# Kernel tuning notes

Hardware: AMD Instinct MI355X
Metric: run time of the kernel (lower is better)

## Reference

```python
import jax, jax.numpy as jnp
import numpy as np

B = 8192
MOTION_DIM = 512
COMMAND_DIM = 64
HIDDEN = 1024
E = 8  # num_experts
NUM_LAYERS = 6


def _dense(key, shape, fan_in):
    return jax.random.normal(key, shape, dtype=jnp.float32) * (1.0 / np.sqrt(fan_in))


def setup_inputs() -> dict:
    key = jax.random.key(0)
    ks = jax.random.split(key, 32)
    in_dim = MOTION_DIM + COMMAND_DIM  # 576
    inp = {
        "motion": jax.random.normal(ks[0], (B, MOTION_DIM), dtype=jnp.float32),
        "command": jax.random.normal(ks[1], (B, COMMAND_DIM), dtype=jnp.float32),
        # gating network: in -> H -> H -> E, ELU, softmax
        "g_w1": _dense(ks[2], (in_dim, HIDDEN), in_dim),
        "g_b1": jnp.zeros((HIDDEN,), jnp.float32),
        "g_w2": _dense(ks[3], (HIDDEN, HIDDEN), HIDDEN),
        "g_b2": jnp.zeros((HIDDEN,), jnp.float32),
        "g_w3": _dense(ks[4], (HIDDEN, E), HIDDEN),
        "g_b3": jnp.zeros((E,), jnp.float32),
        # MoE layers: dims [in->H, H->H, H->H, H->H, H->H?, ...] per CMG layout
        "w0": _dense(ks[5], (E, in_dim, HIDDEN), in_dim),
        "b0": jnp.zeros((E, HIDDEN), jnp.float32),
        "w1": _dense(ks[6], (E, HIDDEN, HIDDEN), HIDDEN),
        "b1": jnp.zeros((E, HIDDEN), jnp.float32),
        "w2": _dense(ks[7], (E, HIDDEN, HIDDEN), HIDDEN),
        "b2": jnp.zeros((E, HIDDEN), jnp.float32),
        "w3": _dense(ks[8], (E, HIDDEN, HIDDEN), HIDDEN),
        "b3": jnp.zeros((E, HIDDEN), jnp.float32),
        "w4": _dense(ks[9], (E, HIDDEN, HIDDEN), HIDDEN),
        "b4": jnp.zeros((E, HIDDEN), jnp.float32),
        "w5": _dense(ks[10], (E, HIDDEN, MOTION_DIM), HIDDEN),
        "b5": jnp.zeros((E, MOTION_DIM), jnp.float32),
    }
    return inp


def _moe_layer(x, coeffs, W, b):
    # x: [B, din], coeffs: [B, E], W: [E, din, dout], b: [E, dout]
    # y[b] = sum_e coeffs[b,e] * (x[b] @ W[e] + b[e])
    y = jnp.einsum("be,bi,eio->bo", coeffs, x, W)
    y = y + jnp.einsum("be,eo->bo", coeffs, b)
    return y


def _cmg_forward(motion, command,
                 g_w1, g_b1, g_w2, g_b2, g_w3, g_b3,
                 w0, b0, w1, b1, w2, b2, w3, b3, w4, b4, w5, b5):
    x = jnp.concatenate([motion, command], axis=-1)  # [B, in_dim]
    # gating network
    g = jax.nn.elu(x @ g_w1 + g_b1)
    g = jax.nn.elu(g @ g_w2 + g_b2)
    coeffs = jax.nn.softmax(g @ g_w3 + g_b3, axis=-1)  # [B, E]
    # stacked MoE layers with ELU between all but last
    Ws = [w0, w1, w2, w3, w4, w5]
    bs = [b0, b1, b2, b3, b4, b5]
    for i in range(NUM_LAYERS):
        x = _moe_layer(x, coeffs, Ws[i], bs[i])
        if i < NUM_LAYERS - 1:
            x = jax.nn.elu(x)
    return x  # [B, MOTION_DIM]


def reference(motion, command,
              g_w1, g_b1, g_w2, g_b2, g_w3, g_b3,
              w0, b0, w1, b1, w2, b2, w3, b3, w4, b4, w5, b5):
    return _cmg_forward(motion, command,
                        g_w1, g_b1, g_w2, g_b2, g_w3, g_b3,
                        w0, b0, w1, b1, w2, b2, w3, b3, w4, b4, w5, b5)
```

## Files before the change

### kernel.cpp

```cpp
#include <hip/hip_runtime.h>
#include <hip/hip_bf16.h>

typedef __attribute__((ext_vector_type(8))) short bf16x8;
typedef __attribute__((ext_vector_type(4))) float f32x4;

__device__ __forceinline__ float bf2f(unsigned short u) {
    union { unsigned int i; float f; } v; v.i = ((unsigned int)u) << 16; return v.f;
}
__device__ __forceinline__ unsigned short f2bf(float f) {
    union { float f; unsigned int i; } v; v.f = f;
    unsigned int x = v.i;
    return (unsigned short)((x + 0x7FFFu + ((x >> 16) & 1u)) >> 16);
}

__device__ __forceinline__ void gload_lds16(const unsigned short* g, unsigned short* l) {
    __builtin_amdgcn_global_load_lds(
        (const __attribute__((address_space(1))) unsigned int*)g,
        (__attribute__((address_space(3))) unsigned int*)l,
        16, 0, 0);
}

#define VM0  asm volatile("s_waitcnt vmcnt(0)" ::: "memory")
#define SB0  __builtin_amdgcn_sched_barrier(0)
#define BAR  __builtin_amdgcn_s_barrier()

__global__ void concat_cvt(const float* __restrict__ motion,
                           const float* __restrict__ command,
                           unsigned short* __restrict__ out) {
    int id = blockIdx.x * 256 + threadIdx.x;
    int b = id / 144, q = id % 144;
    float4 v;
    if (q < 128) v = *(const float4*)(motion + (size_t)b * 512 + q * 4);
    else         v = *(const float4*)(command + (size_t)b * 64 + (q - 128) * 4);
    ushort4 o;
    o.x = f2bf(v.x); o.y = f2bf(v.y); o.z = f2bf(v.z); o.w = f2bf(v.w);
    *(ushort4*)(out + (size_t)b * 576 + q * 4) = o;
}

__global__ void transpose_cvt(const float* __restrict__ in,
                              unsigned short* __restrict__ out,
                              int K, int N, int tpe) {
    __shared__ unsigned short tile[64][72];
    int e = blockIdx.x / tpe, r = blockIdx.x % tpe;
    in  += (size_t)e * K * N;
    out += (size_t)e * N * K;
    int nbn = N / 64;
    int k0 = (r / nbn) * 64;
    int n0 = (r % nbn) * 64;
    int t = threadIdx.x;
    int tx = t & 63, ty = t >> 6;
    #pragma unroll
    for (int rr = 0; rr < 16; ++rr) {
        int kr = ty + rr * 4;
        tile[kr][tx] = f2bf(in[(size_t)(k0 + kr) * N + n0 + tx]);
    }
    __syncthreads();
    int txh = t & 31, tyh = t >> 5;
    #pragma unroll
    for (int rr = 0; rr < 8; ++rr) {
        int nr = tyh + rr * 8;
        unsigned int vlo = tile[2 * txh][nr];
        unsigned int vhi = tile[2 * txh + 1][nr];
        unsigned int* o32 = (unsigned int*)(out + (size_t)(n0 + nr) * K + k0);
        o32[txh] = vlo | (vhi << 16);
    }
}

__global__ __launch_bounds__(256) void gating_kernel(
    const unsigned short* __restrict__ g2,
    const float* __restrict__ w3, const float* __restrict__ b3,
    float* __restrict__ coeffs) {
    __shared__ float w3s[8][1024];
    int t = threadIdx.x;
    for (int i = t; i < 1024; i += 256) {
        #pragma unroll
        for (int e = 0; e < 8; ++e) w3s[e][i] = w3[(size_t)i * 8 + e];
    }
    __syncthreads();
    int lane = t & 63, wv = t >> 6;
    int row = blockIdx.x * 4 + wv;
    const unsigned short* xr = g2 + (size_t)row * 1024;
    float acc[8];
    #pragma unroll
    for (int e = 0; e < 8; ++e) acc[e] = 0.f;
    for (int it = 0; it < 16; ++it) {
        float xv = bf2f(xr[lane + it * 64]);
        #pragma unroll
        for (int e = 0; e < 8; ++e) acc[e] += xv * w3s[e][lane + it * 64];
    }
    #pragma unroll
    for (int e = 0; e < 8; ++e) {
        float v = acc[e];
        #pragma unroll
        for (int off = 32; off; off >>= 1) v += __shfl_xor(v, off);
        acc[e] = v + b3[e];
    }
    float mx = acc[0];
    #pragma unroll
    for (int e = 1; e < 8; ++e) mx = fmaxf(mx, acc[e]);
    float s = 0.f;
    #pragma unroll
    for (int e = 0; e < 8; ++e) { acc[e] = __expf(acc[e] - mx); s += acc[e]; }
    float inv = 1.f / s;
    if (lane < 8) coeffs[(size_t)row * 8 + lane] = acc[lane] * inv;
}

template<bool DO_ELU>
__global__ __launch_bounds__(256, 4)
void gemm_bf16(const unsigned short* __restrict__ A,
               const unsigned short* __restrict__ BT,
               const float* __restrict__ bias,
               unsigned short* __restrict__ Out,
               int N, int ld, int kpart) {
    __shared__ unsigned short As[128 * 64];
    __shared__ unsigned short Bs[128 * 64];
    int ntn = N >> 7;
    int nwg = gridDim.x;
    int bid = blockIdx.x;
    { int cpx = nwg >> 3; bid = (bid & 7) * cpx + (bid >> 3); }
    int tm = bid / ntn, tn = bid - tm * ntn;
    int row0 = tm << 7, col0 = tn << 7;
    int t = threadIdx.x;
    int lane = t & 63;
    int wid = t >> 6;
    int wr = wid >> 1, wc = wid & 1;
    const unsigned short* Ab = A + (size_t)(row0 + wid * 32 + (lane >> 3)) * ld + (lane & 7) * 8;
    const unsigned short* Bb = BT + (size_t)(col0 + wid * 32 + (lane >> 3)) * ld + (lane & 7) * 8;
    unsigned short* Asd = &As[wid * 32 * 64];
    unsigned short* Bsd = &Bs[wid * 32 * 64];
    f32x4 acc[4][4];
    #pragma unroll
    for (int i = 0; i < 4; ++i)
        #pragma unroll
        for (int j = 0; j < 4; ++j) acc[i][j] = (f32x4){0.f, 0.f, 0.f, 0.f};
    int nkt = kpart >> 6;
    for (int kt = 0; kt < nkt; ++kt) {
        size_t ko = (size_t)kt << 6;
        #pragma unroll
        for (int q = 0; q < 4; ++q) {
            gload_lds16(Ab + (size_t)(q * 8) * ld + ko, Asd + q * 8 * 64);
            gload_lds16(Bb + (size_t)(q * 8) * ld + ko, Bsd + q * 8 * 64);
        }
        __syncthreads();
        #pragma unroll
        for (int kk = 0; kk < 2; ++kk) {
            bf16x8 af[4], bfr[4];
            #pragma unroll
            for (int m = 0; m < 4; ++m)
                af[m] = *(const bf16x8*)(&As[(wr * 64 + m * 16 + (lane & 15)) * 64 + kk * 32 + (lane >> 4) * 8]);
            #pragma unroll
            for (int n = 0; n < 4; ++n)
                bfr[n] = *(const bf16x8*)(&Bs[(wc * 64 + n * 16 + (lane & 15)) * 64 + kk * 32 + (lane >> 4) * 8]);
            #pragma unroll
            for (int m = 0; m < 4; ++m)
                #pragma unroll
                for (int n = 0; n < 4; ++n)
                    acc[m][n] = __builtin_amdgcn_mfma_f32_16x16x32_bf16(af[m], bfr[n], acc[m][n], 0, 0, 0);
        }
        __syncthreads();
    }
    #pragma unroll
    for (int m = 0; m < 4; ++m) {
        int rbase = row0 + wr * 64 + m * 16 + ((lane >> 4) << 2);
        #pragma unroll
        for (int n = 0; n < 4; ++n) {
            int cg = col0 + wc * 64 + n * 16 + (lane & 15);
            float bv = bias[cg];
            #pragma unroll
            for (int r2 = 0; r2 < 4; ++r2) {
                float v = acc[m][n][r2] + bv;
                if (DO_ELU) v = v > 0.f ? v : (__expf(v) - 1.f);
                Out[(size_t)(rbase + r2) * N + cg] = f2bf(v);
            }
        }
    }
}

template<bool DO_ELU, bool OUT_F32>
__global__ __launch_bounds__(512, 1)
void gemm_fused(const unsigned short* __restrict__ A,
                const unsigned short* __restrict__ BT,
                const float* __restrict__ coeffs,
                const float* __restrict__ bias,
                void* __restrict__ Out,
                int K, int dout) {
    __shared__ unsigned short lds[65536];

    int bid = blockIdx.x;
    int x = bid & 7;
    int i = bid >> 3;
    int within = i & 15;
    int tm = x * 4 + (within & 3);
    int tn = (i >> 4) * 4 + (within >> 2);
    int row0 = tm << 8;
    int c0 = tn << 5;
    int nkt = K >> 5;

    int t = threadIdx.x;
    int lane = t & 63, wid = t >> 6;
    int wm = wid >> 2, wn = wid & 3;
    int q = lane >> 4;
    int l15 = lane & 15;

    int aoff[8], boff[4];
    #pragma unroll
    for (int m = 0; m < 8; ++m) {
        int row = wm * 128 + m * 16 + l15;
        aoff[m] = row * 32 + ((q ^ ((row >> 1) & 3)) << 3);
    }
    #pragma unroll
    for (int n = 0; n < 4; ++n) {
        int row = wn * 64 + n * 16 + l15;
        boff[n] = 8192 + row * 32 + ((q ^ ((row >> 1) & 3)) << 3);
    }

    int srow = t >> 2;
    int scol = ((t & 3) ^ ((t >> 3) & 3)) * 8;
    const unsigned short* Asrc = A + (size_t)(row0 + srow) * K + scol;
    int br0 = (srow >> 5) * dout + c0 + (srow & 31);
    int br1 = ((srow + 128) >> 5) * dout + c0 + (srow & 31);
    const unsigned short* Bsrc0 = BT + (size_t)br0 * K + scol;
    const unsigned short* Bsrc1 = BT + (size_t)br1 * K + scol;
    int wdst = wid * 512;

    f32x4 acc[8][4];
    #pragma unroll
    for (int m = 0; m < 8; ++m)
        #pragma unroll
        for (int n = 0; n < 4; ++n) acc[m][n] = (f32x4){0.f, 0.f, 0.f, 0.f};

    #pragma unroll
    for (int S = 0; S < 2; ++S) {
        gload_lds16(Asrc + S * 32,                   &lds[S * 16384 + wdst]);
        gload_lds16(Asrc + (size_t)128 * K + S * 32, &lds[S * 16384 + 4096 + wdst]);
        gload_lds16(Bsrc0 + S * 32,                  &lds[S * 16384 + 8192 + wdst]);
        gload_lds16(Bsrc1 + S * 32,                  &lds[S * 16384 + 12288 + wdst]);
    }

    for (int s = 0; s < nkt; s += 2) {
        int sbA = (s & 3) << 14;
        int sbB = ((s + 1) & 3) << 14;
        bool st = (s + 2) < nkt;

        VM0; SB0;
        BAR;
        if (st) {
            int rbA = ((s + 2) & 3) << 14;
            int rbB = ((s + 3) & 3) << 14;
            int koA = (s + 2) << 5;
            int koB = (s + 3) << 5;
            gload_lds16(Asrc + koA,                   &lds[rbA + wdst]);
            gload_lds16(Asrc + (size_t)128 * K + koA, &lds[rbA + 4096 + wdst]);
            gload_lds16(Bsrc0 + koA,                  &lds[rbA + 8192 + wdst]);
            gload_lds16(Bsrc1 + koA,                  &lds[rbA + 12288 + wdst]);
            gload_lds16(Asrc + koB,                   &lds[rbB + wdst]);
            gload_lds16(Asrc + (size_t)128 * K + koB, &lds[rbB + 4096 + wdst]);
            gload_lds16(Bsrc0 + koB,                  &lds[rbB + 8192 + wdst]);
            gload_lds16(Bsrc1 + koB,                  &lds[rbB + 12288 + wdst]);
        }
        SB0;

        {
            bf16x8 bfrg[4], afr[8];
            #pragma unroll
            for (int n = 0; n < 4; ++n)
                bfrg[n] = *(const bf16x8*)(&lds[sbA + boff[n]]);
            #pragma unroll
            for (int m = 0; m < 8; ++m)
                afr[m] = *(const bf16x8*)(&lds[sbA + aoff[m]]);
            __builtin_amdgcn_s_setprio(1);
            #pragma unroll
            for (int m = 0; m < 8; ++m)
                #pragma unroll
                for (int n = 0; n < 4; ++n)
                    acc[m][n] = __builtin_amdgcn_mfma_f32_16x16x32_bf16(bfrg[n], afr[m], acc[m][n], 0, 0, 0);
            __builtin_amdgcn_s_setprio(0);
        }
        {
            bf16x8 bfrg[4], afr[8];
            #pragma unroll
            for (int n = 0; n < 4; ++n)
                bfrg[n] = *(const bf16x8*)(&lds[sbB + boff[n]]);
            #pragma unroll
            for (int m = 0; m < 8; ++m)
                afr[m] = *(const bf16x8*)(&lds[sbB + aoff[m]]);
            __builtin_amdgcn_s_setprio(1);
            #pragma unroll
            for (int m = 0; m < 8; ++m)
                #pragma unroll
                for (int n = 0; n < 4; ++n)
                    acc[m][n] = __builtin_amdgcn_mfma_f32_16x16x32_bf16(bfrg[n], afr[m], acc[m][n], 0, 0, 0);
            __builtin_amdgcn_s_setprio(0);
        }
        SB0;
    }

    float* plds = (float*)lds;
    __syncthreads();
    {
        int e0 = 2 * wn, e1 = e0 + 1;
        f32x4 b0h[2], b1h[2];
        #pragma unroll
        for (int h = 0; h < 2; ++h) {
            float4 u0 = *(const float4*)(bias + e0 * dout + c0 + h * 16 + q * 4);
            float4 u1 = *(const float4*)(bias + e1 * dout + c0 + h * 16 + q * 4);
            b0h[h] = (f32x4){u0.x, u0.y, u0.z, u0.w};
            b1h[h] = (f32x4){u1.x, u1.y, u1.z, u1.w};
        }
        float* preg = plds + (wid << 12);
        #pragma unroll
        for (int m = 0; m < 8; ++m) {
            int grow = row0 + wm * 128 + m * 16 + l15;
            float c8 = coeffs[(size_t)grow * 8 + e0];
            float c9 = coeffs[(size_t)grow * 8 + e1];
            #pragma unroll
            for (int h = 0; h < 2; ++h) {
                f32x4 z0 = acc[m][h];
                f32x4 z1 = acc[m][h + 2];
                f32x4 p;
                #pragma unroll
                for (int r = 0; r < 4; ++r)
                    p[r] = c8 * (z0[r] + b0h[h][r]) + c9 * (z1[r] + b1h[h][r]);
                int row = m * 16 + l15;
                int slot = (h * 4 + q) ^ (row & 7);
                *(f32x4*)(preg + row * 32 + (slot << 2)) = p;
            }
        }
    }
    __syncthreads();

    {
        int r2 = t >> 1;
        int ch = t & 1;
        int wmr = r2 >> 7;
        int rr = r2 & 127;
        int sw = rr & 7;
        size_t obase = (size_t)(row0 + r2) * dout + c0 + ch * 16;
        #pragma unroll
        for (int sl = 0; sl < 4; ++sl) {
            int L = ch * 4 + sl;
            int phys = L ^ sw;
            f32x4 sum = (f32x4){0.f, 0.f, 0.f, 0.f};
            #pragma unroll
            for (int w2 = 0; w2 < 4; ++w2) {
                const f32x4 v = *(const f32x4*)(plds + (((wmr << 2) + w2) << 12) + rr * 32 + (phys << 2));
                sum[0] += v[0]; sum[1] += v[1]; sum[2] += v[2]; sum[3] += v[3];
            }
            if (DO_ELU) {
                #pragma unroll
                for (int r = 0; r < 4; ++r)
                    sum[r] = sum[r] > 0.f ? sum[r] : (__expf(sum[r]) - 1.f);
            }
            if (OUT_F32) {
                float4 o = {sum[0], sum[1], sum[2], sum[3]};
                *(float4*)((float*)Out + obase + sl * 4) = o;
            } else {
                ushort4 o;
                o.x = f2bf(sum[0]); o.y = f2bf(sum[1]);
                o.z = f2bf(sum[2]); o.w = f2bf(sum[3]);
                *(ushort4*)((unsigned short*)Out + obase + sl * 4) = o;
            }
        }
    }
}

extern "C" void kernel_launch(void* const* d_in, const int* in_sizes, int n_in,
                              void* d_out, int out_size, void* d_ws, size_t ws_size,
                              hipStream_t stream) {
    const float* motion  = (const float*)d_in[0];
    const float* command = (const float*)d_in[1];
    const float* g_w1 = (const float*)d_in[2];
    const float* g_b1 = (const float*)d_in[3];
    const float* g_w2 = (const float*)d_in[4];
    const float* g_b2 = (const float*)d_in[5];
    const float* g_w3 = (const float*)d_in[6];
    const float* g_b3 = (const float*)d_in[7];
    const float* w[6]  = {(const float*)d_in[8],  (const float*)d_in[10],
                          (const float*)d_in[12], (const float*)d_in[14],
                          (const float*)d_in[16], (const float*)d_in[18]};
    const float* bb[6] = {(const float*)d_in[9],  (const float*)d_in[11],
                          (const float*)d_in[13], (const float*)d_in[15],
                          (const float*)d_in[17], (const float*)d_in[19]};

    char* ws = (char*)d_ws;
    unsigned short* xc0  = (unsigned short*)ws;
    unsigned short* actA = (unsigned short*)(ws + 9437184);
    unsigned short* actB = (unsigned short*)(ws + 26214400);
    float* coeffs        = (float*)(ws + 42991616);
    unsigned short* wT   = (unsigned short*)(ws + 43253760);

    concat_cvt<<<4608, 256, 0, stream>>>(motion, command, xc0);

    transpose_cvt<<<144, 256, 0, stream>>>(g_w1, wT, 576, 1024, 144);
    gemm_bf16<true><<<512, 256, 0, stream>>>(xc0, wT, g_b1, actA, 1024, 576, 576);
    transpose_cvt<<<256, 256, 0, stream>>>(g_w2, wT, 1024, 1024, 256);
    gemm_bf16<true><<<512, 256, 0, stream>>>(actA, wT, g_b2, actB, 1024, 1024, 1024);
    gating_kernel<<<2048, 256, 0, stream>>>(actB, g_w3, g_b3, coeffs);

    transpose_cvt<<<1152, 256, 0, stream>>>(w[0], wT, 576, 1024, 144);
    gemm_fused<true, false><<<1024, 512, 0, stream>>>(
        xc0, wT, coeffs, bb[0], actA, 576, 1024);

    unsigned short* bufs[2] = {actA, actB};
    for (int l = 1; l <= 4; ++l) {
        unsigned short* in  = bufs[(l + 1) & 1];
        unsigned short* out = bufs[l & 1];
        transpose_cvt<<<2048, 256, 0, stream>>>(w[l], wT, 1024, 1024, 256);
        gemm_fused<true, false><<<1024, 512, 0, stream>>>(
            in, wT, coeffs, bb[l], out, 1024, 1024);
    }

    transpose_cvt<<<1024, 256, 0, stream>>>(w[5], wT, 1024, 512, 128);
    gemm_fused<false, true><<<512, 512, 0, stream>>>(
        actA, wT, coeffs, bb[5], d_out, 1024, 512);
}
```

Before: 736.0 us.

## Load B fragments directly to registers and pipeline A through LDS per k-step

The B operand (expert weight tiles) is now read straight from global memory into registers in MFMA fragment layout, double-buffered across k-steps, rather than staged through LDS. Only A tiles are still staged in LDS, using a 4-slot ring with partial vmcnt waits and one barrier per 32-wide k-step instead of full drains every two steps. This cuts LDS traffic and space for B and lets loads overlap compute more finely. In exchange it adds more frequent barriers, uncoalesced per-lane 16-byte global reads for B, and higher register pressure.

```diff
diff --git a/kernel.cpp b/kernel.cpp
--- a/kernel.cpp
+++ b/kernel.cpp
@@ -20,6 +20,8 @@
         16, 0, 0);
 }
 
+#define VM2  asm volatile("s_waitcnt vmcnt(2)" ::: "memory")
+#define VM6  asm volatile("s_waitcnt vmcnt(6)" ::: "memory")
 #define VM0  asm volatile("s_waitcnt vmcnt(0)" ::: "memory")
 #define SB0  __builtin_amdgcn_sched_barrier(0)
 #define BAR  __builtin_amdgcn_s_barrier()
@@ -202,98 +204,87 @@
     int q = lane >> 4;
     int l15 = lane & 15;
 
-    int aoff[8], boff[4];
+    int aoff[8];
     #pragma unroll
     for (int m = 0; m < 8; ++m) {
         int row = wm * 128 + m * 16 + l15;
         aoff[m] = row * 32 + ((q ^ ((row >> 1) & 3)) << 3);
     }
-    #pragma unroll
-    for (int n = 0; n < 4; ++n) {
-        int row = wn * 64 + n * 16 + l15;
-        boff[n] = 8192 + row * 32 + ((q ^ ((row >> 1) & 3)) << 3);
-    }
 
     int srow = t >> 2;
     int scol = ((t & 3) ^ ((t >> 3) & 3)) * 8;
     const unsigned short* Asrc = A + (size_t)(row0 + srow) * K + scol;
-    int br0 = (srow >> 5) * dout + c0 + (srow & 31);
-    int br1 = ((srow + 128) >> 5) * dout + c0 + (srow & 31);
-    const unsigned short* Bsrc0 = BT + (size_t)br0 * K + scol;
-    const unsigned short* Bsrc1 = BT + (size_t)br1 * K + scol;
     int wdst = wid * 512;
 
+    const unsigned short* Bp[4];
+    #pragma unroll
+    for (int n = 0; n < 4; ++n) {
+        int e = 2 * wn + (n >> 1);
+        int j = (n & 1) * 16 + l15;
+        Bp[n] = BT + (size_t)(e * dout + c0 + j) * K + q * 8;
+    }
+
     f32x4 acc[8][4];
     #pragma unroll
     for (int m = 0; m < 8; ++m)
         #pragma unroll
         for (int n = 0; n < 4; ++n) acc[m][n] = (f32x4){0.f, 0.f, 0.f, 0.f};
 
-    #pragma unroll
-    for (int S = 0; S < 2; ++S) {
-        gload_lds16(Asrc + S * 32,                   &lds[S * 16384 + wdst]);
-        gload_lds16(Asrc + (size_t)128 * K + S * 32, &lds[S * 16384 + 4096 + wdst]);
-        gload_lds16(Bsrc0 + S * 32,                  &lds[S * 16384 + 8192 + wdst]);
-        gload_lds16(Bsrc1 + S * 32,                  &lds[S * 16384 + 12288 + wdst]);
+    uint4 bA0, bA1, bA2, bA3, bB0, bB1, bB2, bB3;
+
+    gload_lds16(Asrc,                    &lds[wdst]);
+    gload_lds16(Asrc + (size_t)128 * K,  &lds[4096 + wdst]);
+    gload_lds16(Asrc + 32,                   &lds[8192 + wdst]);
+    gload_lds16(Asrc + (size_t)128 * K + 32, &lds[8192 + 4096 + wdst]);
+    bA0 = *(const uint4*)(Bp[0]);
+    bA1 = *(const uint4*)(Bp[1]);
+    bA2 = *(const uint4*)(Bp[2]);
+    bA3 = *(const uint4*)(Bp[3]);
+    VM6; SB0;
+    BAR;
+
+    #define SLOT_BODY(S, CUR0, CUR1, CUR2, CUR3, NX0, NX1, NX2, NX3)            \
+    {                                                                           \
+        int s_ = (S);                                                           \
+        bool st_ = (s_ + 2) < nkt;                                              \
+        if (st_) {                                                              \
+            int rb_ = ((s_ + 2) & 3) << 13;                                     \
+            int ko_ = (s_ + 2) << 5;                                            \
+            gload_lds16(Asrc + ko_,                   &lds[rb_ + wdst]);        \
+            gload_lds16(Asrc + (size_t)128 * K + ko_, &lds[rb_ + 4096 + wdst]); \
+        }                                                                       \
+        if (st_) { VM2; } else { VM0; }                                         \
+        BAR; SB0;                                                               \
+        if ((s_ + 1) < nkt) {                                                   \
+            int kb_ = (s_ + 1) << 5;                                            \
+            NX0 = *(const uint4*)(Bp[0] + kb_);                                 \
+            NX1 = *(const uint4*)(Bp[1] + kb_);                                 \
+            NX2 = *(const uint4*)(Bp[2] + kb_);                                 \
+            NX3 = *(const uint4*)(Bp[3] + kb_);                                 \
+        }                                                                       \
+        int sb_ = (s_ & 3) << 13;                                               \
+        bf16x8 afr_[8];                                                         \
+        _Pragma("unroll")                                                       \
+        for (int m = 0; m < 8; ++m)                                             \
+            afr_[m] = *(const bf16x8*)(&lds[sb_ + aoff[m]]);                    \
+        bf16x8 bf0_ = *(const bf16x8*)&CUR0;                                    \
+        bf16x8 bf1_ = *(const bf16x8*)&CUR1;                                    \
+        bf16x8 bf2_ = *(const bf16x8*)&CUR2;                                    \
+        bf16x8 bf3_ = *(const bf16x8*)&CUR3;                                    \
+        _Pragma("unroll")                                                       \
+        for (int m = 0; m < 8; ++m) {                                           \
+            acc[m][0] = __builtin_amdgcn_mfma_f32_16x16x32_bf16(bf0_, afr_[m], acc[m][0], 0, 0, 0); \
+            acc[m][1] = __builtin_amdgcn_mfma_f32_16x16x32_bf16(bf1_, afr_[m], acc[m][1], 0, 0, 0); \
+            acc[m][2] = __builtin_amdgcn_mfma_f32_16x16x32_bf16(bf2_, afr_[m], acc[m][2], 0, 0, 0); \
+            acc[m][3] = __builtin_amdgcn_mfma_f32_16x16x32_bf16(bf3_, afr_[m], acc[m][3], 0, 0, 0); \
+        }                                                                       \
     }
 
     for (int s = 0; s < nkt; s += 2) {
-        int sbA = (s & 3) << 14;
-        int sbB = ((s + 1) & 3) << 14;
-        bool st = (s + 2) < nkt;
-
-        VM0; SB0;
-        BAR;
-        if (st) {
-            int rbA = ((s + 2) & 3) << 14;
-            int rbB = ((s + 3) & 3) << 14;
-            int koA = (s + 2) << 5;
-            int koB = (s + 3) << 5;
-            gload_lds16(Asrc + koA,                   &lds[rbA + wdst]);
-            gload_lds16(Asrc + (size_t)128 * K + koA, &lds[rbA + 4096 + wdst]);
-            gload_lds16(Bsrc0 + koA,                  &lds[rbA + 8192 + wdst]);
-            gload_lds16(Bsrc1 + koA,                  &lds[rbA + 12288 + wdst]);
-            gload_lds16(Asrc + koB,                   &lds[rbB + wdst]);
-            gload_lds16(Asrc + (size_t)128 * K + koB, &lds[rbB + 4096 + wdst]);
-            gload_lds16(Bsrc0 + koB,                  &lds[rbB + 8192 + wdst]);
-            gload_lds16(Bsrc1 + koB,                  &lds[rbB + 12288 + wdst]);
-        }
-        SB0;
-
-        {
-            bf16x8 bfrg[4], afr[8];
-            #pragma unroll
-            for (int n = 0; n < 4; ++n)
-                bfrg[n] = *(const bf16x8*)(&lds[sbA + boff[n]]);
-            #pragma unroll
-            for (int m = 0; m < 8; ++m)
-                afr[m] = *(const bf16x8*)(&lds[sbA + aoff[m]]);
-            __builtin_amdgcn_s_setprio(1);
-            #pragma unroll
-            for (int m = 0; m < 8; ++m)
-                #pragma unroll
-                for (int n = 0; n < 4; ++n)
-                    acc[m][n] = __builtin_amdgcn_mfma_f32_16x16x32_bf16(bfrg[n], afr[m], acc[m][n], 0, 0, 0);
-            __builtin_amdgcn_s_setprio(0);
-        }
-        {
-            bf16x8 bfrg[4], afr[8];
-            #pragma unroll
-            for (int n = 0; n < 4; ++n)
-                bfrg[n] = *(const bf16x8*)(&lds[sbB + boff[n]]);
-            #pragma unroll
-            for (int m = 0; m < 8; ++m)
-                afr[m] = *(const bf16x8*)(&lds[sbB + aoff[m]]);
-            __builtin_amdgcn_s_setprio(1);
-            #pragma unroll
-            for (int m = 0; m < 8; ++m)
-                #pragma unroll
-                for (int n = 0; n < 4; ++n)
-                    acc[m][n] = __builtin_amdgcn_mfma_f32_16x16x32_bf16(bfrg[n], afr[m], acc[m][n], 0, 0, 0);
-            __builtin_amdgcn_s_setprio(0);
-        }
-        SB0;
-    }
+        SLOT_BODY(s,     bA0, bA1, bA2, bA3, bB0, bB1, bB2, bB3);
+        SLOT_BODY(s + 1, bB0, bB1, bB2, bB3, bA0, bA1, bA2, bA3);
+    }
+    #undef SLOT_BODY
 
     float* plds = (float*)lds;
     __syncthreads();
```

New measurement: 1.076 ms. 46.1% more time.
